# Kernel tuning notes

Measured on AMD Instinct MI355X. Metric: run time of the kernel, lower is better.

## Reference

```python
import jax, jax.numpy as jnp
import numpy as np

N_NODES = 100000
N_EDGES = 1600000
NUM_FEAT = 64
DIM = 32
K = 3  # num_stacks
T = 2  # num_layers


def setup_inputs() -> dict:
    key = jax.random.key(0)
    ks = jax.random.split(key, 10)
    g = lambda k, s, fan: jax.random.normal(k, s, jnp.float32) * (1.0 / np.sqrt(fan))
    x = jax.random.normal(ks[0], (N_NODES, NUM_FEAT), jnp.float32)
    edge_index = jax.random.randint(ks[1], (2, N_EDGES), 0, N_NODES)
    return {
        "x": x,
        "edge_index": edge_index,
        "w1_init": g(ks[2], (K, NUM_FEAT, DIM), NUM_FEAT),
        "w1": g(ks[3], (1, K, DIM, DIM), DIM),
        "w1_root": g(ks[4], (1, K, NUM_FEAT, DIM), NUM_FEAT),
        "b1": jnp.zeros((1, K, 1, DIM), jnp.float32),
        "w2_init": g(ks[5], (K, DIM, DIM), DIM),
        "w2": g(ks[6], (1, K, DIM, DIM), DIM),
        "w2_root": g(ks[7], (1, K, DIM, DIM), DIM),
        "b2": jnp.zeros((1, K, 1, DIM), jnp.float32),
    }


def _gcn_norm(src, dst, num_nodes):
    # symmetric normalization WITHOUT self loops (PyG ARMAConv default)
    deg = jax.ops.segment_sum(jnp.ones(src.shape[0], jnp.float32), dst, num_segments=num_nodes)
    dinv = jnp.where(deg > 0, jax.lax.rsqrt(jnp.maximum(deg, 1.0)), 0.0)
    return dinv[src] * dinv[dst]  # [E]


def _arma_conv(x, src, dst, norm, init_w, w, root_w, b, act):
    # x: [N,F_in]; init_w: [K,F_in,F_out]; w/root_w/b: shared (leading dim 1)
    num_nodes = x.shape[0]
    out = jnp.einsum('nf,kfo->kno', x, init_w)          # [K,N,F_out]
    root_term = jnp.einsum('nf,kfo->kno', x, root_w[0])  # shared across layers
    bias = b[0]                                          # [K,1,F_out]

    def prop(o):  # o: [N,F_out] -> A_hat @ o
        return jax.ops.segment_sum(o[src] * norm[:, None], dst, num_segments=num_nodes)

    for t in range(T):
        if t > 0:
            out = jnp.einsum('knf,kfo->kno', out, w[0])
        out = jax.vmap(prop)(out)
        out = act(out + root_term + bias)
    return out.mean(axis=0)  # mean over stacks -> [N,F_out]


def reference(x, edge_index, w1_init, w1, w1_root, b1, w2_init, w2, w2_root, b2):
    src, dst = edge_index[0], edge_index[1]
    norm = _gcn_norm(src, dst, x.shape[0])
    # eval mode: dropout is identity
    h = jax.nn.relu(_arma_conv(x, src, dst, norm, w1_init, w1, w1_root, b1, jax.nn.relu))
    out = _arma_conv(h, src, dst, norm, w2_init, w2, w2_root, b2, lambda z: z)
    return out
```

## Files before the change

kernel.cpp:

```cpp
#include <hip/hip_runtime.h>
#include <hip/hip_bf16.h>


#define KSTACK 3
#define DIM    32
#define FDIM   96
#define NB     256
#define TILE   4096

typedef __hip_bfloat16 bf16;
typedef _Float16 f16;
typedef _Float16 halfx2 __attribute__((ext_vector_type(2)));

__device__ __forceinline__ float dot2h(unsigned int a, unsigned int b, float c) {
#if __has_builtin(__builtin_amdgcn_fdot2)
    return __builtin_amdgcn_fdot2(__builtin_bit_cast(halfx2, a),
                                  __builtin_bit_cast(halfx2, b), c, false);
#else
    halfx2 ha = __builtin_bit_cast(halfx2, a);
    halfx2 hb = __builtin_bit_cast(halfx2, b);
    return c + (float)ha.x * (float)hb.x + (float)ha.y * (float)hb.y;
#endif
}

__device__ __forceinline__ unsigned int pkh(float lo, float hi) {
    return __builtin_bit_cast(unsigned int, __builtin_amdgcn_cvt_pkrtz(lo, hi));
}

__device__ __forceinline__ halfx2 h2(unsigned int q) {
    return __builtin_bit_cast(halfx2, q);
}


__global__ void zero_int_kernel(int* __restrict__ p, int n) {
    int i = blockIdx.x * 256 + threadIdx.x;
    if (i < n) p[i] = 0;
}

__global__ __launch_bounds__(256) void bucket_hist_kernel(const int* __restrict__ dst,
                                                          int* __restrict__ bcnt, int E) {
    __shared__ int cnt[NB];
    for (int i = threadIdx.x; i < NB; i += 256) cnt[i] = 0;
    __syncthreads();
    const int e0 = blockIdx.x * TILE;
    const int count = min(TILE, E - e0);
    for (int u = threadIdx.x; u < count; u += 256)
        atomicAdd(&cnt[dst[e0 + u] >> 9], 1);
    __syncthreads();
    for (int i = threadIdx.x; i < NB; i += 256)
        if (cnt[i]) atomicAdd(&bcnt[i], cnt[i]);
}

__global__ __launch_bounds__(256) void bucket_scan_kernel(const int* __restrict__ bcnt,
                                                          int* __restrict__ gcur,
                                                          int* __restrict__ gbase) {
    __shared__ int s[NB];
    const int t = threadIdx.x;
    int v = bcnt[t];
    s[t] = v;
    __syncthreads();
    for (int off = 1; off < NB; off <<= 1) {
        int add = (t >= off) ? s[t - off] : 0;
        __syncthreads();
        s[t] += add;
        __syncthreads();
    }
    gcur[t]  = s[t] - v;
    gbase[t] = s[t] - v;
}

__global__ __launch_bounds__(256) void group_edges_kernel(
    const int* __restrict__ src, const int* __restrict__ dst,
    int* __restrict__ gcur, int2* __restrict__ grouped, int E)
{
    __shared__ int cnt[NB], pref[NB], lbase[NB], lofs[NB], gres[NB];
    __shared__ int2 stage[TILE];
    const int tid = threadIdx.x;
    const int e0 = blockIdx.x * TILE;
    const int count = min(TILE, E - e0);
    cnt[tid] = 0;
    __syncthreads();
    #pragma unroll
    for (int u = 0; u < TILE / 256; ++u) {
        int idx = u * 256 + tid;
        if (idx < count) atomicAdd(&cnt[dst[e0 + idx] >> 9], 1);
    }
    __syncthreads();
    int v = cnt[tid];
    pref[tid] = v;
    __syncthreads();
    for (int off = 1; off < NB; off <<= 1) {
        int add = (tid >= off) ? pref[tid - off] : 0;
        __syncthreads();
        pref[tid] += add;
        __syncthreads();
    }
    int ex = pref[tid] - v;
    lbase[tid] = ex;
    lofs[tid]  = ex;
    gres[tid] = atomicAdd(&gcur[tid], v);
    __syncthreads();
    #pragma unroll
    for (int u = 0; u < TILE / 256; ++u) {
        int idx = u * 256 + tid;
        if (idx < count) {
            int e = e0 + idx;
            int d = dst[e];
            int lp = atomicAdd(&lofs[d >> 9], 1);
            stage[lp] = make_int2(src[e] << 6, d);
        }
    }
    __syncthreads();
    for (int i = tid; i < count; i += 256) {
        int2 pr = stage[i];
        int b = pr.y >> 9;
        grouped[gres[b] + (i - lbase[b])] = pr;
    }
}

__global__ __launch_bounds__(256) void deg_from_grouped_kernel(
    const int2* __restrict__ grouped, const int* __restrict__ gbase,
    const int* __restrict__ bcnt, int* __restrict__ deg, int N)
{
    __shared__ int h[512];
    const int b  = blockIdx.x;
    const int nb = b * 512;
    for (int i = threadIdx.x; i < 512; i += 256) h[i] = 0;
    __syncthreads();
    const int e0 = gbase[b], cnt = bcnt[b];
    for (int u = threadIdx.x; u < cnt; u += 256)
        atomicAdd(&h[grouped[e0 + u].y & 511], 1);
    __syncthreads();
    for (int i = threadIdx.x; i < 512; i += 256)
        if (nb + i < N) deg[nb + i] = h[i];
}

__global__ void dinv_kernel(const int* __restrict__ deg, float* __restrict__ dinv, int N) {
    int i = blockIdx.x * 256 + threadIdx.x;
    if (i < N) {
        int d = deg[i];
        dinv[i] = (d > 0) ? rsqrtf((float)d) : 0.0f;
    }
}

__global__ __launch_bounds__(512) void scan1_kernel(const int* __restrict__ deg,
                                                    int* __restrict__ off4,
                                                    int* __restrict__ bsums, int N) {
    __shared__ int tmp[512];
    int t = threadIdx.x;
    int i = blockIdx.x * 512 + t;
    int v = (i < N) ? ((deg[i] + 3) & ~3) : 0;
    tmp[t] = v;
    __syncthreads();
    for (int off = 1; off < 512; off <<= 1) {
        int add = (t >= off) ? tmp[t - off] : 0;
        __syncthreads();
        tmp[t] += add;
        __syncthreads();
    }
    if (i <= N) off4[i] = tmp[t] - v;
    if (t == 511) bsums[blockIdx.x] = tmp[511];
}

__global__ void scan2_kernel(int* __restrict__ bsums, int nb) {
    if (blockIdx.x == 0 && threadIdx.x == 0) {
        int run = 0;
        for (int b = 0; b < nb; ++b) { int v = bsums[b]; bsums[b] = run; run += v; }
    }
}

__global__ void scan3_kernel(int* __restrict__ off4, const int* __restrict__ bsums, int N) {
    int i = blockIdx.x * 256 + threadIdx.x;
    if (i <= N) off4[i] += bsums[i >> 9];
}

__global__ __launch_bounds__(256) void fill_csr_bucket_kernel(
    const int2* __restrict__ grouped, const int* __restrict__ gbase,
    const int* __restrict__ bcnt, const int* __restrict__ off4,
    int* __restrict__ csr, int N, int dummy)
{
    __shared__ int lofs[512];
    const int b  = blockIdx.x;
    const int nb = b * 512;
    for (int i = threadIdx.x; i < 512; i += 256)
        lofs[i] = (nb + i < N) ? off4[nb + i] : 0;
    __syncthreads();
    const int e0 = gbase[b], cnt = bcnt[b];
    for (int u = threadIdx.x; u < cnt; u += 256) {
        int2 pr = grouped[e0 + u];
        int pos = atomicAdd(&lofs[pr.y & 511], 1);
        csr[pos] = pr.x;
    }
    __syncthreads();
    for (int i = threadIdx.x; i < 512; i += 256) {
        int n = nb + i;
        if (n < N) {
            int p = lofs[i];
            int e = off4[n + 1];
            for (; p < e; ++p) csr[p] = dummy;
        }
    }
}

__global__ void zero_dummy_kernel(f16* __restrict__ a, f16* __restrict__ b,
                                  f16* __restrict__ c, int N) {
    int t = threadIdx.x;
    if (t < FDIM) {
        a[(long)N * FDIM + t] = (f16)0.f;
        b[(long)N * FDIM + t] = (f16)0.f;
    }
    if (t < DIM) c[(long)N * DIM + t] = (f16)0.f;
}


__device__ __forceinline__ unsigned int f2bf_bits(float v) {
    unsigned int u = __float_as_uint(v);
    return (u + 0x7fffu + ((u >> 16) & 1u)) >> 16;
}

template <int FIN, bool MEANROOT>
__global__ __launch_bounds__(256) void mm_init_kernel(
    const float* __restrict__ x,
    const float* __restrict__ wA,
    const float* __restrict__ wB,
    const float* __restrict__ dinv,
    f16*   __restrict__ outA,
    f16*   __restrict__ rootb,
    float* __restrict__ rootm,
    const float* __restrict__ bias,
    int N)
{
    constexpr int NW = KSTACK * FIN * 32;
    __shared__ unsigned int swAB[NW];
    __shared__ float sx[FIN * 68];
    const int tid = threadIdx.x;
    const int n0  = blockIdx.x * 64;

    for (int i = tid; i < NW; i += 256)
        swAB[i] = f2bf_bits(wA[i]) | (f2bf_bits(wB[i]) << 16);
    for (int i = tid; i < 64 * FIN; i += 256) {
        int jj = i / FIN, f = i % FIN;
        int n = n0 + jj; if (n >= N) n = N - 1;
        sx[f * 68 + jj] = x[(long)n * FIN + f];
    }
    __syncthreads();

    const int o = tid & 31;
    const int g = tid >> 5;
    float bz[KSTACK];
    #pragma unroll
    for (int k = 0; k < KSTACK; ++k) bz[k] = bias[k * 32 + o];
    float accA[8][KSTACK];
    float accB[8][KSTACK];
    #pragma unroll
    for (int jj = 0; jj < 8; ++jj)
        #pragma unroll
        for (int k = 0; k < KSTACK; ++k) { accA[jj][k] = 0.f; accB[jj][k] = 0.f; }

    #pragma unroll 2
    for (int f = 0; f < FIN; ++f) {
        float4 xlo = *reinterpret_cast<const float4*>(&sx[f * 68 + 8 * g]);
        float4 xhi = *reinterpret_cast<const float4*>(&sx[f * 68 + 8 * g + 4]);
        float xv[8] = {xlo.x, xlo.y, xlo.z, xlo.w, xhi.x, xhi.y, xhi.z, xhi.w};
        #pragma unroll
        for (int k = 0; k < KSTACK; ++k) {
            unsigned int q = swAB[(k * FIN + f) * 32 + o];
            float wa = __uint_as_float(q << 16);
            float wb = __uint_as_float(q & 0xffff0000u);
            #pragma unroll
            for (int jj = 0; jj < 8; ++jj) {
                accA[jj][k] += xv[jj] * wa;
                accB[jj][k] += xv[jj] * wb;
            }
        }
    }

    #pragma unroll
    for (int jj = 0; jj < 8; ++jj) {
        long n = n0 + 8 * g + jj;
        if (n < N) {
            const float di = dinv[n];
            float rsum = 0.f;
            #pragma unroll
            for (int k = 0; k < KSTACK; ++k) {
                float rb = accB[jj][k] + bz[k];
                outA[n * FDIM + k * 32 + o]  = (f16)(accA[jj][k] * di);
                rootb[n * FDIM + k * 32 + o] = (f16)rb;
                rsum += rb;
            }
            if (MEANROOT)
                rootm[n * 32 + o] = rsum * (1.0f / 3.0f);
        }
    }
}


#define GATHER_LOOP8()                                                         \
    const int m = max(nA, nB);                                                 \
    halfx2 aA01a = {0, 0}, aA23a = {0, 0}, aA01b = {0, 0}, aA23b = {0, 0};     \
    halfx2 aB01a = {0, 0}, aB23a = {0, 0}, aB01b = {0, 0}, aB23b = {0, 0};     \
    for (int b = 0; b < m; b += 8) {                                           \
        int4 tA0 = *reinterpret_cast<const int4*>(csr + iA + b);               \
        int4 tA1 = *reinterpret_cast<const int4*>(csr + iA + b + 4);           \
        int4 tB0 = *reinterpret_cast<const int4*>(csr + iB + b);               \
        int4 tB1 = *reinterpret_cast<const int4*>(csr + iB + b + 4);           \
        const int rA = nA - b, rB = nB - b;                                    \
        int oA0 = rA > 0 ? tA0.x : dummy;                                      \
        int oA1 = rA > 1 ? tA0.y : dummy;                                      \
        int oA2 = rA > 2 ? tA0.z : dummy;                                      \
        int oA3 = rA > 3 ? tA0.w : dummy;                                      \
        int oA4 = rA > 4 ? tA1.x : dummy;                                      \
        int oA5 = rA > 5 ? tA1.y : dummy;                                      \
        int oA6 = rA > 6 ? tA1.z : dummy;                                      \
        int oA7 = rA > 7 ? tA1.w : dummy;                                      \
        int oB0 = rB > 0 ? tB0.x : dummy;                                      \
        int oB1 = rB > 1 ? tB0.y : dummy;                                      \
        int oB2 = rB > 2 ? tB0.z : dummy;                                      \
        int oB3 = rB > 3 ? tB0.w : dummy;                                      \
        int oB4 = rB > 4 ? tB1.x : dummy;                                      \
        int oB5 = rB > 5 ? tB1.y : dummy;                                      \
        int oB6 = rB > 6 ? tB1.z : dummy;                                      \
        int oB7 = rB > 7 ? tB1.w : dummy;                                      \
        if (ld) {                                                              \
            uint2 qA0 = *reinterpret_cast<const uint2*>(base + 3 * oA0 + lb);  \
            uint2 qA1 = *reinterpret_cast<const uint2*>(base + 3 * oA1 + lb);  \
            uint2 qA2 = *reinterpret_cast<const uint2*>(base + 3 * oA2 + lb);  \
            uint2 qA3 = *reinterpret_cast<const uint2*>(base + 3 * oA3 + lb);  \
            uint2 qA4 = *reinterpret_cast<const uint2*>(base + 3 * oA4 + lb);  \
            uint2 qA5 = *reinterpret_cast<const uint2*>(base + 3 * oA5 + lb);  \
            uint2 qA6 = *reinterpret_cast<const uint2*>(base + 3 * oA6 + lb);  \
            uint2 qA7 = *reinterpret_cast<const uint2*>(base + 3 * oA7 + lb);  \
            uint2 qB0 = *reinterpret_cast<const uint2*>(base + 3 * oB0 + lb);  \
            uint2 qB1 = *reinterpret_cast<const uint2*>(base + 3 * oB1 + lb);  \
            uint2 qB2 = *reinterpret_cast<const uint2*>(base + 3 * oB2 + lb);  \
            uint2 qB3 = *reinterpret_cast<const uint2*>(base + 3 * oB3 + lb);  \
            uint2 qB4 = *reinterpret_cast<const uint2*>(base + 3 * oB4 + lb);  \
            uint2 qB5 = *reinterpret_cast<const uint2*>(base + 3 * oB5 + lb);  \
            uint2 qB6 = *reinterpret_cast<const uint2*>(base + 3 * oB6 + lb);  \
            uint2 qB7 = *reinterpret_cast<const uint2*>(base + 3 * oB7 + lb);  \
            aA01a += h2(qA0.x); aA23a += h2(qA0.y);                            \
            aA01b += h2(qA1.x); aA23b += h2(qA1.y);                            \
            aA01a += h2(qA2.x); aA23a += h2(qA2.y);                            \
            aA01b += h2(qA3.x); aA23b += h2(qA3.y);                            \
            aA01a += h2(qA4.x); aA23a += h2(qA4.y);                            \
            aA01b += h2(qA5.x); aA23b += h2(qA5.y);                            \
            aA01a += h2(qA6.x); aA23a += h2(qA6.y);                            \
            aA01b += h2(qA7.x); aA23b += h2(qA7.y);                            \
            aB01a += h2(qB0.x); aB23a += h2(qB0.y);                            \
            aB01b += h2(qB1.x); aB23b += h2(qB1.y);                            \
            aB01a += h2(qB2.x); aB23a += h2(qB2.y);                            \
            aB01b += h2(qB3.x); aB23b += h2(qB3.y);                            \
            aB01a += h2(qB4.x); aB23a += h2(qB4.y);                            \
            aB01b += h2(qB5.x); aB23b += h2(qB5.y);                            \
            aB01a += h2(qB6.x); aB23a += h2(qB6.y);                            \
            aB01b += h2(qB7.x); aB23b += h2(qB7.y);                            \
        }                                                                      \
    }                                                                          \
    const float aA0 = (float)aA01a.x + (float)aA01b.x;                         \
    const float aA1 = (float)aA01a.y + (float)aA01b.y;                         \
    const float aA2 = (float)aA23a.x + (float)aA23b.x;                         \
    const float aA3 = (float)aA23a.y + (float)aA23b.y;                         \
    const float aB0 = (float)aB01a.x + (float)aB01b.x;                         \
    const float aB1 = (float)aB01a.y + (float)aB01b.y;                         \
    const float aB2 = (float)aB23a.x + (float)aB23b.x;                         \
    const float aB3 = (float)aB23a.y + (float)aB23b.y;

#define DST_SETUP()                                                            \
    const int dA = blockIdx.x * 16 + j;                                        \
    const int dB = dA + 8;                                                     \
    const bool vA = dA < N, vB = dB < N;                                       \
    const int dummy = N * 64;                                                  \
    const bool ld  = lane < 24;                                                \
    const int  lb  = lane * 8;                                                 \
    const char* base = (const char*)in;                                        \
    halfx2 rA01 = {0, 0}, rA23 = {0, 0}, rB01 = {0, 0}, rB23 = {0, 0};         \
    int iA = 0, nA = 0, iB = 0, nB = 0;                                        \
    float diA = 0.f, diB = 0.f;                                                \
    if (vA) {                                                                  \
        iA = off4[dA]; nA = off4[dA + 1] - iA; diA = dinv[dA];                 \
        if (ld) {                                                              \
            uint2 rr = *reinterpret_cast<const uint2*>(                        \
                (const char*)root + (long)dA * 192 + lb);                      \
            rA01 = h2(rr.x); rA23 = h2(rr.y);                                  \
        }                                                                      \
    }                                                                          \
    if (vB) {                                                                  \
        iB = off4[dB]; nB = off4[dB + 1] - iB; diB = dinv[dB];                 \
        if (ld) {                                                              \
            uint2 rr = *reinterpret_cast<const uint2*>(                        \
                (const char*)root + (long)dB * 192 + lb);                      \
            rB01 = h2(rr.x); rB23 = h2(rr.y);                                  \
        }                                                                      \
    }

__device__ __forceinline__ void gemv96(const unsigned int* __restrict__ sv,
                                       const unsigned int* __restrict__ sw2,
                                       int lane, float& r0, float& r1, float& r2) {
    float o[KSTACK];
    #pragma unroll
    for (int k = 0; k < KSTACK; ++k) {
        const unsigned int* sp = sv + k * 16;
        uint4 s0 = *reinterpret_cast<const uint4*>(sp);
        uint4 s1 = *reinterpret_cast<const uint4*>(sp + 4);
        uint4 s2 = *reinterpret_cast<const uint4*>(sp + 8);
        uint4 s3 = *reinterpret_cast<const uint4*>(sp + 12);
        const unsigned int* wp = sw2 + k * 512 + lane;
        float a = 0.f;
        a = dot2h(s0.x, wp[0],   a); a = dot2h(s0.y, wp[32],  a);
        a = dot2h(s0.z, wp[64],  a); a = dot2h(s0.w, wp[96],  a);
        a = dot2h(s1.x, wp[128], a); a = dot2h(s1.y, wp[160], a);
        a = dot2h(s1.z, wp[192], a); a = dot2h(s1.w, wp[224], a);
        a = dot2h(s2.x, wp[256], a); a = dot2h(s2.y, wp[288], a);
        a = dot2h(s2.z, wp[320], a); a = dot2h(s2.w, wp[352], a);
        a = dot2h(s3.x, wp[384], a); a = dot2h(s3.y, wp[416], a);
        a = dot2h(s3.z, wp[448], a); a = dot2h(s3.w, wp[480], a);
        o[k] = a;
    }
    r0 = o[0]; r1 = o[1]; r2 = o[2];
}

__global__ __launch_bounds__(256) void prop_mm_kernel(
    const f16*   __restrict__ in,
    const int*   __restrict__ off4,
    const int*   __restrict__ csr,
    const float* __restrict__ dinv,
    const f16*   __restrict__ root,
    const float* __restrict__ w,
    f16* __restrict__ out, int N)
{
    __shared__ unsigned int sw2[KSTACK * 512];
    __shared__ unsigned int sv2[16][48];
    const int tid = threadIdx.x;
    for (int i = tid; i < KSTACK * 512; i += 256) {
        int k = i >> 9, r = i & 511, t = r >> 5, o = r & 31;
        sw2[i] = pkh(w[(k * 32 + 2 * t) * 32 + o], w[(k * 32 + 2 * t + 1) * 32 + o]);
    }
    __syncthreads();
    const int lane = tid & 31;
    const int j    = tid >> 5;
    DST_SETUP();

    GATHER_LOOP8();

    if (ld) {
        if (vA) {
            float v0 = fmaxf(aA0 * diA + (float)rA01.x, 0.f);
            float v1 = fmaxf(aA1 * diA + (float)rA01.y, 0.f);
            float v2 = fmaxf(aA2 * diA + (float)rA23.x, 0.f);
            float v3 = fmaxf(aA3 * diA + (float)rA23.y, 0.f);
            sv2[j][2 * lane]     = pkh(v0, v1);
            sv2[j][2 * lane + 1] = pkh(v2, v3);
        }
        if (vB) {
            float v0 = fmaxf(aB0 * diB + (float)rB01.x, 0.f);
            float v1 = fmaxf(aB1 * diB + (float)rB01.y, 0.f);
            float v2 = fmaxf(aB2 * diB + (float)rB23.x, 0.f);
            float v3 = fmaxf(aB3 * diB + (float)rB23.y, 0.f);
            sv2[j + 8][2 * lane]     = pkh(v0, v1);
            sv2[j + 8][2 * lane + 1] = pkh(v2, v3);
        }
    }
    if (vA) {
        float o0, o1, o2;
        gemv96(&sv2[j][0], sw2, lane, o0, o1, o2);
        out[(long)dA * FDIM + lane]      = (f16)(o0 * diA);
        out[(long)dA * FDIM + 32 + lane] = (f16)(o1 * diA);
        out[(long)dA * FDIM + 64 + lane] = (f16)(o2 * diA);
    }
    if (vB) {
        float o0, o1, o2;
        gemv96(&sv2[j + 8][0], sw2, lane, o0, o1, o2);
        out[(long)dB * FDIM + lane]      = (f16)(o0 * diB);
        out[(long)dB * FDIM + 32 + lane] = (f16)(o1 * diB);
        out[(long)dB * FDIM + 64 + lane] = (f16)(o2 * diB);
    }
}

__global__ __launch_bounds__(256) void prop_mean_kernel(
    const f16*   __restrict__ in,
    const int*   __restrict__ off4,
    const int*   __restrict__ csr,
    const float* __restrict__ dinv,
    const f16*   __restrict__ root,
    float* __restrict__ out,
    int N)
{
    __shared__ float sv[16][FDIM];
    const int tid = threadIdx.x;
    const int lane = tid & 31;
    const int j    = tid >> 5;
    DST_SETUP();

    GATHER_LOOP8();

    if (ld) {
        if (vA) {
            sv[j][4*lane]   = fmaxf(aA0 * diA + (float)rA01.x, 0.f);
            sv[j][4*lane+1] = fmaxf(aA1 * diA + (float)rA01.y, 0.f);
            sv[j][4*lane+2] = fmaxf(aA2 * diA + (float)rA23.x, 0.f);
            sv[j][4*lane+3] = fmaxf(aA3 * diA + (float)rA23.y, 0.f);
        }
        if (vB) {
            sv[j+8][4*lane]   = fmaxf(aB0 * diB + (float)rB01.x, 0.f);
            sv[j+8][4*lane+1] = fmaxf(aB1 * diB + (float)rB01.y, 0.f);
            sv[j+8][4*lane+2] = fmaxf(aB2 * diB + (float)rB23.x, 0.f);
            sv[j+8][4*lane+3] = fmaxf(aB3 * diB + (float)rB23.y, 0.f);
        }
    }
    if (vA) {
        float mv = fmaxf((sv[j][lane] + sv[j][32 + lane] + sv[j][64 + lane]) * (1.0f / 3.0f), 0.f);
        out[(long)dA * 32 + lane] = mv;
    }
    if (vB) {
        float mv = fmaxf((sv[j+8][lane] + sv[j+8][32 + lane] + sv[j+8][64 + lane]) * (1.0f / 3.0f), 0.f);
        out[(long)dB * 32 + lane] = mv;
    }
}

__global__ __launch_bounds__(256) void prop_mm_mean_kernel(
    const f16*   __restrict__ in,
    const int*   __restrict__ off4,
    const int*   __restrict__ csr,
    const float* __restrict__ dinv,
    const f16*   __restrict__ root,
    const float* __restrict__ w,
    f16* __restrict__ out, int N)
{
    __shared__ unsigned int sw2[KSTACK * 512];
    __shared__ unsigned int sv2[16][48];
    const int tid = threadIdx.x;
    for (int i = tid; i < KSTACK * 512; i += 256) {
        int k = i >> 9, r = i & 511, t = r >> 5, o = r & 31;
        sw2[i] = pkh(w[(k * 32 + 2 * t) * 32 + o], w[(k * 32 + 2 * t + 1) * 32 + o]);
    }
    __syncthreads();
    const int lane = tid & 31;
    const int j    = tid >> 5;
    DST_SETUP();

    GATHER_LOOP8();

    if (ld) {
        if (vA) {
            sv2[j][2 * lane]     = pkh(aA0 * diA + (float)rA01.x, aA1 * diA + (float)rA01.y);
            sv2[j][2 * lane + 1] = pkh(aA2 * diA + (float)rA23.x, aA3 * diA + (float)rA23.y);
        }
        if (vB) {
            sv2[j + 8][2 * lane]     = pkh(aB0 * diB + (float)rB01.x, aB1 * diB + (float)rB01.y);
            sv2[j + 8][2 * lane + 1] = pkh(aB2 * diB + (float)rB23.x, aB3 * diB + (float)rB23.y);
        }
    }
    if (vA) {
        float o0, o1, o2;
        gemv96(&sv2[j][0], sw2, lane, o0, o1, o2);
        out[(long)dA * 32 + lane] = (f16)((o0 + o1 + o2) * (diA * (1.0f / 3.0f)));
    }
    if (vB) {
        float o0, o1, o2;
        gemv96(&sv2[j + 8][0], sw2, lane, o0, o1, o2);
        out[(long)dB * 32 + lane] = (f16)((o0 + o1 + o2) * (diB * (1.0f / 3.0f)));
    }
}

__global__ __launch_bounds__(256) void prop_mean2_kernel(
    const f16*   __restrict__ in,
    const int*   __restrict__ off4,
    const int*   __restrict__ csr,
    const float* __restrict__ dinv,
    const float* __restrict__ rootm,
    float* __restrict__ out,
    int N)
{
    const int lane = threadIdx.x & 15;
    const int g    = threadIdx.x >> 4;
    const int d    = blockIdx.x * 16 + g;
    if (d >= N) return;
    const int dummy = N * 64;
    const int lb = lane * 4;
    const char* base = (const char*)in;
    const int i0 = off4[d];
    const int n  = off4[d + 1] - i0;
    halfx2 aa = {0, 0}, ab = {0, 0};
    for (int b = 0; b < n; b += 8) {
        int4 t0 = *reinterpret_cast<const int4*>(csr + i0 + b);
        int4 t1 = *reinterpret_cast<const int4*>(csr + i0 + b + 4);
        const int r = n - b;
        int o0 = r > 0 ? t0.x : dummy;
        int o1 = r > 1 ? t0.y : dummy;
        int o2 = r > 2 ? t0.z : dummy;
        int o3 = r > 3 ? t0.w : dummy;
        int o4 = r > 4 ? t1.x : dummy;
        int o5 = r > 5 ? t1.y : dummy;
        int o6 = r > 6 ? t1.z : dummy;
        int o7 = r > 7 ? t1.w : dummy;
        unsigned int q0 = *reinterpret_cast<const unsigned int*>(base + o0 + lb);
        unsigned int q1 = *reinterpret_cast<const unsigned int*>(base + o1 + lb);
        unsigned int q2 = *reinterpret_cast<const unsigned int*>(base + o2 + lb);
        unsigned int q3 = *reinterpret_cast<const unsigned int*>(base + o3 + lb);
        unsigned int q4 = *reinterpret_cast<const unsigned int*>(base + o4 + lb);
        unsigned int q5 = *reinterpret_cast<const unsigned int*>(base + o5 + lb);
        unsigned int q6 = *reinterpret_cast<const unsigned int*>(base + o6 + lb);
        unsigned int q7 = *reinterpret_cast<const unsigned int*>(base + o7 + lb);
        aa += h2(q0); ab += h2(q1); aa += h2(q2); ab += h2(q3);
        aa += h2(q4); ab += h2(q5); aa += h2(q6); ab += h2(q7);
    }
    const float di = dinv[d];
    float a0 = (float)aa.x + (float)ab.x;
    float a1 = (float)aa.y + (float)ab.y;
    float2 rm = *reinterpret_cast<const float2*>(rootm + (long)d * 32 + 2 * lane);
    float2 res = make_float2(a0 * di + rm.x, a1 * di + rm.y);
    *reinterpret_cast<float2*>(out + (long)d * 32 + 2 * lane) = res;
}


extern "C" void kernel_launch(void* const* d_in, const int* in_sizes, int n_in,
                              void* d_out, int out_size, void* d_ws, size_t ws_size,
                              hipStream_t stream) {
    const float* x       = (const float*)d_in[0];
    const int*   edge    = (const int*)  d_in[1];
    const float* w1_init = (const float*)d_in[2];
    const float* w1      = (const float*)d_in[3];
    const float* w1_root = (const float*)d_in[4];
    const float* b1      = (const float*)d_in[5];
    const float* w2_init = (const float*)d_in[6];
    const float* w2      = (const float*)d_in[7];
    const float* w2_root = (const float*)d_in[8];
    const float* b2      = (const float*)d_in[9];
    float* out = (float*)d_out;

    const int N = in_sizes[0] / 64;
    const int E = in_sizes[1] / 2;
    const int* src = edge;
    const int* dst = edge + E;
    const int E4max = E + 3 * N;

    char* p = (char*)d_ws;
    auto alloc = [&](size_t bytes) { void* r = (void*)p; p += (bytes + 255) & ~(size_t)255; return r; };
    int*   deg      = (int*)  alloc((size_t)N * 4);
    float* dinv     = (float*)alloc((size_t)N * 4);
    int*   off4     = (int*)  alloc((size_t)(N + 1) * 4);
    const int nScanBlocks = (N + 1 + 511) / 512;
    int*   bsums    = (int*)  alloc((size_t)nScanBlocks * 4);
    int*   bcnt     = (int*)  alloc((size_t)NB * 4);
    int*   gcur     = (int*)  alloc((size_t)NB * 4);
    int*   gbase    = (int*)  alloc((size_t)NB * 4);
    int*   csr_boff = (int*)  alloc((size_t)(E4max + 1024) * 4);
    f16*   gatherA  = (f16*)  alloc((size_t)(N + 1) * FDIM * 2);
    f16*   gatherB  = (f16*)  alloc((size_t)(N + 1) * FDIM * 2);
    f16*   grow2    = (f16*)  alloc((size_t)(N + 1) * DIM * 2);
    f16*   rootb    = (f16*)  alloc((size_t)N * FDIM * 2);
    float* rootm    = (float*)alloc((size_t)N * DIM * 4);
    float* hbuf     = (float*)alloc((size_t)N * DIM * 4);
    int2*  grouped  = (int2*) alloc((size_t)E * 8);
    (void)ws_size; (void)n_in; (void)out_size;

    const int gN     = (N + 255) / 256;
    const int gN1    = (N + 1 + 255) / 256;
    const int gT     = (E + TILE - 1) / TILE;
    const int gNod64 = (N + 63) / 64;
    const int gNod16 = (N + 15) / 16;

    zero_int_kernel<<<1, 256, 0, stream>>>(bcnt, NB);
    bucket_hist_kernel<<<gT, 256, 0, stream>>>(dst, bcnt, E);
    bucket_scan_kernel<<<1, NB, 0, stream>>>(bcnt, gcur, gbase);
    group_edges_kernel<<<gT, 256, 0, stream>>>(src, dst, gcur, grouped, E);
    deg_from_grouped_kernel<<<NB, 256, 0, stream>>>(grouped, gbase, bcnt, deg, N);
    dinv_kernel<<<gN, 256, 0, stream>>>(deg, dinv, N);
    scan1_kernel<<<nScanBlocks, 512, 0, stream>>>(deg, off4, bsums, N);
    scan2_kernel<<<1, 64, 0, stream>>>(bsums, nScanBlocks);
    scan3_kernel<<<gN1, 256, 0, stream>>>(off4, bsums, N);
    fill_csr_bucket_kernel<<<NB, 256, 0, stream>>>(grouped, gbase, bcnt, off4, csr_boff, N, N * 64);
    zero_dummy_kernel<<<1, 96, 0, stream>>>(gatherA, gatherB, grow2, N);

    mm_init_kernel<64, false><<<gNod64, 256, 0, stream>>>(x, w1_init, w1_root, dinv, gatherA, rootb, nullptr, b1, N);
    prop_mm_kernel<<<gNod16, 256, 0, stream>>>(gatherA, off4, csr_boff, dinv, rootb, w1, gatherB, N);
    prop_mean_kernel<<<gNod16, 256, 0, stream>>>(gatherB, off4, csr_boff, dinv, rootb, hbuf, N);

    mm_init_kernel<32, true><<<gNod64, 256, 0, stream>>>(hbuf, w2_init, w2_root, dinv, gatherA, rootb, rootm, b2, N);
    prop_mm_mean_kernel<<<gNod16, 256, 0, stream>>>(gatherA, off4, csr_boff, dinv, rootb, w2, grow2, N);
    prop_mean2_kernel<<<gNod16, 256, 0, stream>>>(grow2, off4, csr_boff, dinv, rootm, out, N);
}
```

Before: 375.8 us.

## Use fp16 dot2 in init GEMM, fp16 hidden buffer, unroll gather to 16

New measurement: 396.1 us. 1.05x slower.

```diff
diff --git a/kernel.cpp b/kernel.cpp
--- a/kernel.cpp
+++ b/kernel.cpp
@@ -213,14 +213,10 @@
 }
 
 
-__device__ __forceinline__ unsigned int f2bf_bits(float v) {
-    unsigned int u = __float_as_uint(v);
-    return (u + 0x7fffu + ((u >> 16) & 1u)) >> 16;
-}
-
-template <int FIN, bool MEANROOT>
+template <int FIN, bool MEANROOT, bool XF16>
 __global__ __launch_bounds__(256) void mm_init_kernel(
-    const float* __restrict__ x,
+    const float* __restrict__ xf,
+    const f16*   __restrict__ xh,
     const float* __restrict__ wA,
     const float* __restrict__ wB,
     const float* __restrict__ dinv,
@@ -230,18 +226,25 @@
     const float* __restrict__ bias,
     int N)
 {
-    constexpr int NW = KSTACK * FIN * 32;
-    __shared__ unsigned int swAB[NW];
-    __shared__ float sx[FIN * 68];
+    constexpr int F2 = FIN / 2;
+    __shared__ unsigned int swA2[KSTACK * F2 * 32];
+    __shared__ unsigned int swB2[KSTACK * F2 * 32];
+    __shared__ unsigned int sx2[F2 * 64];
     const int tid = threadIdx.x;
     const int n0  = blockIdx.x * 64;
 
-    for (int i = tid; i < NW; i += 256)
-        swAB[i] = f2bf_bits(wA[i]) | (f2bf_bits(wB[i]) << 16);
-    for (int i = tid; i < 64 * FIN; i += 256) {
-        int jj = i / FIN, f = i % FIN;
+    for (int i = tid; i < KSTACK * F2 * 32; i += 256) {
+        int k = i / (F2 * 32), r = i % (F2 * 32), f2 = r >> 5, o = r & 31;
+        swA2[i] = pkh(wA[(k * FIN + 2 * f2) * 32 + o], wA[(k * FIN + 2 * f2 + 1) * 32 + o]);
+        swB2[i] = pkh(wB[(k * FIN + 2 * f2) * 32 + o], wB[(k * FIN + 2 * f2 + 1) * 32 + o]);
+    }
+    for (int i = tid; i < 64 * F2; i += 256) {
+        int jj = i / F2, f2 = i % F2;
         int n = n0 + jj; if (n >= N) n = N - 1;
-        sx[f * 68 + jj] = x[(long)n * FIN + f];
+        unsigned int v;
+        if (XF16) v = *reinterpret_cast<const unsigned int*>(xh + (long)n * FIN + 2 * f2);
+        else      v = pkh(xf[(long)n * FIN + 2 * f2], xf[(long)n * FIN + 2 * f2 + 1]);
+        sx2[f2 * 64 + jj] = v;
     }
     __syncthreads();
 
@@ -258,19 +261,18 @@
         for (int k = 0; k < KSTACK; ++k) { accA[jj][k] = 0.f; accB[jj][k] = 0.f; }
 
     #pragma unroll 2
-    for (int f = 0; f < FIN; ++f) {
-        float4 xlo = *reinterpret_cast<const float4*>(&sx[f * 68 + 8 * g]);
-        float4 xhi = *reinterpret_cast<const float4*>(&sx[f * 68 + 8 * g + 4]);
-        float xv[8] = {xlo.x, xlo.y, xlo.z, xlo.w, xhi.x, xhi.y, xhi.z, xhi.w};
+    for (int f2 = 0; f2 < F2; ++f2) {
+        uint4 xlo = *reinterpret_cast<const uint4*>(&sx2[f2 * 64 + 8 * g]);
+        uint4 xhi = *reinterpret_cast<const uint4*>(&sx2[f2 * 64 + 8 * g + 4]);
+        unsigned int xp[8] = {xlo.x, xlo.y, xlo.z, xlo.w, xhi.x, xhi.y, xhi.z, xhi.w};
         #pragma unroll
         for (int k = 0; k < KSTACK; ++k) {
-            unsigned int q = swAB[(k * FIN + f) * 32 + o];
-            float wa = __uint_as_float(q << 16);
-            float wb = __uint_as_float(q & 0xffff0000u);
+            unsigned int wa2 = swA2[(k * F2 + f2) * 32 + o];
+            unsigned int wb2 = swB2[(k * F2 + f2) * 32 + o];
             #pragma unroll
             for (int jj = 0; jj < 8; ++jj) {
-                accA[jj][k] += xv[jj] * wa;
-                accB[jj][k] += xv[jj] * wb;
+                accA[jj][k] = dot2h(xp[jj], wa2, accA[jj][k]);
+                accB[jj][k] = dot2h(xp[jj], wb2, accB[jj][k]);
             }
         }
     }
@@ -295,65 +297,66 @@
 }
 
 
-#define GATHER_LOOP8()                                                         \
+#define GATHER_LOOP16()                                                        \
     const int m = max(nA, nB);                                                 \
     halfx2 aA01a = {0, 0}, aA23a = {0, 0}, aA01b = {0, 0}, aA23b = {0, 0};     \
     halfx2 aB01a = {0, 0}, aB23a = {0, 0}, aB01b = {0, 0}, aB23b = {0, 0};     \
-    for (int b = 0; b < m; b += 8) {                                           \
+    for (int b = 0; b < m; b += 16) {                                          \
         int4 tA0 = *reinterpret_cast<const int4*>(csr + iA + b);               \
         int4 tA1 = *reinterpret_cast<const int4*>(csr + iA + b + 4);           \
+        int4 tA2 = *reinterpret_cast<const int4*>(csr + iA + b + 8);           \
+        int4 tA3 = *reinterpret_cast<const int4*>(csr + iA + b + 12);          \
         int4 tB0 = *reinterpret_cast<const int4*>(csr + iB + b);               \
         int4 tB1 = *reinterpret_cast<const int4*>(csr + iB + b + 4);           \
+        int4 tB2 = *reinterpret_cast<const int4*>(csr + iB + b + 8);           \
+        int4 tB3 = *reinterpret_cast<const int4*>(csr + iB + b + 12);          \
         const int rA = nA - b, rB = nB - b;                                    \
-        int oA0 = rA > 0 ? tA0.x : dummy;                                      \
-        int oA1 = rA > 1 ? tA0.y : dummy;                                      \
-        int oA2 = rA > 2 ? tA0.z : dummy;                                      \
-        int oA3 = rA > 3 ? tA0.w : dummy;                                      \
-        int oA4 = rA > 4 ? tA1.x : dummy;                                      \
-        int oA5 = rA > 5 ? tA1.y : dummy;                                      \
-        int oA6 = rA > 6 ? tA1.z : dummy;                                      \
-        int oA7 = rA > 7 ? tA1.w : dummy;                                      \
-        int oB0 = rB > 0 ? tB0.x : dummy;                                      \
-        int oB1 = rB > 1 ? tB0.y : dummy;                                      \
-        int oB2 = rB > 2 ? tB0.z : dummy;                                      \
-        int oB3 = rB > 3 ? tB0.w : dummy;                                      \
-        int oB4 = rB > 4 ? tB1.x : dummy;                                      \
-        int oB5 = rB > 5 ? tB1.y : dummy;                                      \
-        int oB6 = rB > 6 ? tB1.z : dummy;                                      \
-        int oB7 = rB > 7 ? tB1.w : dummy;                                      \
+        int oA[16], oB[16];                                                    \
+        oA[0]  = rA > 0  ? tA0.x : dummy;                                      \
+        oA[1]  = rA > 1  ? tA0.y : dummy;                                      \
+        oA[2]  = rA > 2  ? tA0.z : dummy;                                      \
+        oA[3]  = rA > 3  ? tA0.w : dummy;                                      \
+        oA[4]  = rA > 4  ? tA1.x : dummy;                                      \
+        oA[5]  = rA > 5  ? tA1.y : dummy;                                      \
+        oA[6]  = rA > 6  ? tA1.z : dummy;                                      \
+        oA[7]  = rA > 7  ? tA1.w : dummy;                                      \
+        oA[8]  = rA > 8  ? tA2.x : dummy;                                      \
+        oA[9]  = rA > 9  ? tA2.y : dummy;                                      \
+        oA[10] = rA > 10 ? tA2.z : dummy;                                      \
+        oA[11] = rA > 11 ? tA2.w : dummy;                                      \
+        oA[12] = rA > 12 ? tA3.x : dummy;                                      \
+        oA[13] = rA > 13 ? tA3.y : dummy;                                      \
+        oA[14] = rA > 14 ? tA3.z : dummy;                                      \
+        oA[15] = rA > 15 ? tA3.w : dummy;                                      \
+        oB[0]  = rB > 0  ? tB0.x : dummy;                                      \
+        oB[1]  = rB > 1  ? tB0.y : dummy;                                      \
+        oB[2]  = rB > 2  ? tB0.z : dummy;                                      \
+        oB[3]  = rB > 3  ? tB0.w : dummy;                                      \
+        oB[4]  = rB > 4  ? tB1.x : dummy;                                      \
+        oB[5]  = rB > 5  ? tB1.y : dummy;                                      \
+        oB[6]  = rB > 6  ? tB1.z : dummy;                                      \
+        oB[7]  = rB > 7  ? tB1.w : dummy;                                      \
+        oB[8]  = rB > 8  ? tB2.x : dummy;                                      \
+        oB[9]  = rB > 9  ? tB2.y : dummy;                                      \
+        oB[10] = rB > 10 ? tB2.z : dummy;                                      \
+        oB[11] = rB > 11 ? tB2.w : dummy;                                      \
+        oB[12] = rB > 12 ? tB3.x : dummy;                                      \
+        oB[13] = rB > 13 ? tB3.y : dummy;                                      \
+        oB[14] = rB > 14 ? tB3.z : dummy;                                      \
+        oB[15] = rB > 15 ? tB3.w : dummy;                                      \
         if (ld) {                                                              \
-            uint2 qA0 = *reinterpret_cast<const uint2*>(base + 3 * oA0 + lb);  \
-            uint2 qA1 = *reinterpret_cast<const uint2*>(base + 3 * oA1 + lb);  \
-            uint2 qA2 = *reinterpret_cast<const uint2*>(base + 3 * oA2 + lb);  \
-            uint2 qA3 = *reinterpret_cast<const uint2*>(base + 3 * oA3 + lb);  \
-            uint2 qA4 = *reinterpret_cast<const uint2*>(base + 3 * oA4 + lb);  \
-            uint2 qA5 = *reinterpret_cast<const uint2*>(base + 3 * oA5 + lb);  \
-            uint2 qA6 = *reinterpret_cast<const uint2*>(base + 3 * oA6 + lb);  \
-            uint2 qA7 = *reinterpret_cast<const uint2*>(base + 3 * oA7 + lb);  \
-            uint2 qB0 = *reinterpret_cast<const uint2*>(base + 3 * oB0 + lb);  \
-            uint2 qB1 = *reinterpret_cast<const uint2*>(base + 3 * oB1 + lb);  \
-            uint2 qB2 = *reinterpret_cast<const uint2*>(base + 3 * oB2 + lb);  \
-            uint2 qB3 = *reinterpret_cast<const uint2*>(base + 3 * oB3 + lb);  \
-            uint2 qB4 = *reinterpret_cast<const uint2*>(base + 3 * oB4 + lb);  \
-            uint2 qB5 = *reinterpret_cast<const uint2*>(base + 3 * oB5 + lb);  \
-            uint2 qB6 = *reinterpret_cast<const uint2*>(base + 3 * oB6 + lb);  \
-            uint2 qB7 = *reinterpret_cast<const uint2*>(base + 3 * oB7 + lb);  \
-            aA01a += h2(qA0.x); aA23a += h2(qA0.y);                            \
-            aA01b += h2(qA1.x); aA23b += h2(qA1.y);                            \
-            aA01a += h2(qA2.x); aA23a += h2(qA2.y);                            \
-            aA01b += h2(qA3.x); aA23b += h2(qA3.y);                            \
-            aA01a += h2(qA4.x); aA23a += h2(qA4.y);                            \
-            aA01b += h2(qA5.x); aA23b += h2(qA5.y);                            \
-            aA01a += h2(qA6.x); aA23a += h2(qA6.y);                            \
-            aA01b += h2(qA7.x); aA23b += h2(qA7.y);                            \
-            aB01a += h2(qB0.x); aB23a += h2(qB0.y);                            \
-            aB01b += h2(qB1.x); aB23b += h2(qB1.y);                            \
-            aB01a += h2(qB2.x); aB23a += h2(qB2.y);                            \
-            aB01b += h2(qB3.x); aB23b += h2(qB3.y);                            \
-            aB01a += h2(qB4.x); aB23a += h2(qB4.y);                            \
-            aB01b += h2(qB5.x); aB23b += h2(qB5.y);                            \
-            aB01a += h2(qB6.x); aB23a += h2(qB6.y);                            \
-            aB01b += h2(qB7.x); aB23b += h2(qB7.y);                            \
+            _Pragma("unroll")                                                  \
+            for (int t = 0; t < 16; ++t) {                                     \
+                uint2 qa = *reinterpret_cast<const uint2*>(base + 3 * oA[t] + lb); \
+                uint2 qb = *reinterpret_cast<const uint2*>(base + 3 * oB[t] + lb); \
+                if (t & 1) {                                                   \
+                    aA01b += h2(qa.x); aA23b += h2(qa.y);                      \
+                    aB01b += h2(qb.x); aB23b += h2(qb.y);                      \
+                } else {                                                       \
+                    aA01a += h2(qa.x); aA23a += h2(qa.y);                      \
+                    aB01a += h2(qb.x); aB23a += h2(qb.y);                      \
+                }                                                              \
+            }                                                                  \
         }                                                                      \
     }                                                                          \
     const float aA0 = (float)aA01a.x + (float)aA01b.x;                         \
@@ -440,7 +443,7 @@
     const int j    = tid >> 5;
     DST_SETUP();
 
-    GATHER_LOOP8();
+    GATHER_LOOP16();
 
     if (ld) {
         if (vA) {
@@ -482,7 +485,7 @@
     const int*   __restrict__ csr,
     const float* __restrict__ dinv,
     const f16*   __restrict__ root,
-    float* __restrict__ out,
+    f16* __restrict__ out,
     int N)
 {
     __shared__ float sv[16][FDIM];
@@ -491,7 +494,7 @@
     const int j    = tid >> 5;
     DST_SETUP();
 
-    GATHER_LOOP8();
+    GATHER_LOOP16();
 
     if (ld) {
         if (vA) {
@@ -509,11 +512,11 @@
     }
     if (vA) {
         float mv = fmaxf((sv[j][lane] + sv[j][32 + lane] + sv[j][64 + lane]) * (1.0f / 3.0f), 0.f);
-        out[(long)dA * 32 + lane] = mv;
+        out[(long)dA * 32 + lane] = (f16)mv;
     }
     if (vB) {
         float mv = fmaxf((sv[j+8][lane] + sv[j+8][32 + lane] + sv[j+8][64 + lane]) * (1.0f / 3.0f), 0.f);
-        out[(long)dB * 32 + lane] = mv;
+        out[(long)dB * 32 + lane] = (f16)mv;
     }
 }
 
@@ -538,7 +541,7 @@
     const int j    = tid >> 5;
     DST_SETUP();
 
-    GATHER_LOOP8();
+    GATHER_LOOP16();
 
     if (ld) {
         if (vA) {
@@ -650,7 +653,7 @@
     f16*   grow2    = (f16*)  alloc((size_t)(N + 1) * DIM * 2);
     f16*   rootb    = (f16*)  alloc((size_t)N * FDIM * 2);
     float* rootm    = (float*)alloc((size_t)N * DIM * 4);
-    float* hbuf     = (float*)alloc((size_t)N * DIM * 4);
+    f16*   hbuf     = (f16*)  alloc((size_t)N * DIM * 2);
     int2*  grouped  = (int2*) alloc((size_t)E * 8);
     (void)ws_size; (void)n_in; (void)out_size;
 
@@ -672,11 +675,11 @@
     fill_csr_bucket_kernel<<<NB, 256, 0, stream>>>(grouped, gbase, bcnt, off4, csr_boff, N, N * 64);
     zero_dummy_kernel<<<1, 96, 0, stream>>>(gatherA, gatherB, grow2, N);
 
-    mm_init_kernel<64, false><<<gNod64, 256, 0, stream>>>(x, w1_init, w1_root, dinv, gatherA, rootb, nullptr, b1, N);
+    mm_init_kernel<64, false, false><<<gNod64, 256, 0, stream>>>(x, nullptr, w1_init, w1_root, dinv, gatherA, rootb, nullptr, b1, N);
     prop_mm_kernel<<<gNod16, 256, 0, stream>>>(gatherA, off4, csr_boff, dinv, rootb, w1, gatherB, N);
     prop_mean_kernel<<<gNod16, 256, 0, stream>>>(gatherB, off4, csr_boff, dinv, rootb, hbuf, N);
 
-    mm_init_kernel<32, true><<<gNod64, 256, 0, stream>>>(hbuf, w2_init, w2_root, dinv, gatherA, rootb, rootm, b2, N);
+    mm_init_kernel<32, true, true><<<gNod64, 256, 0, stream>>>(nullptr, hbuf, w2_init, w2_root, dinv, gatherA, rootb, rootm, b2, N);
     prop_mm_mean_kernel<<<gNod16, 256, 0, stream>>>(gatherA, off4, csr_boff, dinv, rootb, w2, grow2, N);
     prop_mean2_kernel<<<gNod16, 256, 0, stream>>>(grow2, off4, csr_boff, dinv, rootm, out, N);
 }
```
